# Optimization experiments

Hardware: AMD Instinct MI355X
Metric: run time of the kernel (lower is better)

Reference implementation:

```python
import jax, jax.numpy as jnp
import numpy as np

B, T, D, H = 16, 256, 128, 256  # batch, max_len, input_size, hidden_size (= attention hidden)


def _gru(x_seq, h0, Wih, Whh, bih, bhh):
    """Torch-style GRU over time. x_seq: [B,T,H_in], h0: [B,H]. Returns outputs [B,T,H], hT [B,H]."""
    x_proj = jnp.einsum('bti,gi->btg', x_seq, Wih) + bih  # [B,T,3H], precompute input projections

    def step(h, xp):
        gi_r, gi_z, gi_n = jnp.split(xp, 3, axis=-1)
        gh = h @ Whh.T + bhh
        gh_r, gh_z, gh_n = jnp.split(gh, 3, axis=-1)
        r = jax.nn.sigmoid(gi_r + gh_r)
        z = jax.nn.sigmoid(gi_z + gh_z)
        n = jnp.tanh(gi_n + r * gh_n)
        h_new = (1.0 - z) * n + z * h
        return h_new, h_new

    hT, outs = jax.lax.scan(step, h0, jnp.swapaxes(x_proj, 0, 1))  # scan over time
    return jnp.swapaxes(outs, 0, 1), hT


def setup_inputs() -> dict:
    key = jax.random.key(0)
    ks = jax.random.split(key, 16)
    s = lambda fan: 1.0 / np.sqrt(fan)
    inp = {
        'inputs': jax.random.normal(ks[0], (B, T, D), dtype=jnp.float32),
        'targets': jax.vmap(lambda k: jax.random.permutation(k, T))(jax.random.split(ks[1], B)).astype(jnp.int64),
        'W_enc': jax.random.normal(ks[2], (H, D), dtype=jnp.float32) * s(D),
        'b_enc': jnp.zeros((H,), dtype=jnp.float32),
        'enc_Wih': jax.random.normal(ks[3], (3 * H, H), dtype=jnp.float32) * s(H),
        'enc_Whh': jax.random.normal(ks[4], (3 * H, H), dtype=jnp.float32) * s(H),
        'enc_bih': jnp.zeros((3 * H,), dtype=jnp.float32),
        'enc_bhh': jnp.zeros((3 * H,), dtype=jnp.float32),
        'dec_Wih': jax.random.normal(ks[5], (3 * H, H), dtype=jnp.float32) * s(H),
        'dec_Whh': jax.random.normal(ks[6], (3 * H, H), dtype=jnp.float32) * s(H),
        'dec_bih': jnp.zeros((3 * H,), dtype=jnp.float32),
        'dec_bhh': jnp.zeros((3 * H,), dtype=jnp.float32),
        'Wq': jax.random.normal(ks[7], (H, H), dtype=jnp.float32) * s(H),
        'Wk': jax.random.normal(ks[8], (H, H), dtype=jnp.float32) * s(H),
        'v': jax.random.normal(ks[9], (H,), dtype=jnp.float32) * s(H),
    }
    return inp


def reference(inputs, targets, W_enc, b_enc, enc_Wih, enc_Whh, enc_bih, enc_bhh,
              dec_Wih, dec_Whh, dec_bih, dec_bhh, Wq, Wk, v):
    # encoder_linear (dropout = 0 at inference)
    enc_in = jnp.einsum('btd,hd->bth', inputs, W_enc) + b_enc  # [B,T,H]
    enc_out, hT = _gru(enc_in, jnp.zeros((B, H), dtype=inputs.dtype), enc_Wih, enc_Whh, enc_bih, enc_bhh)
    # teacher forcing: decoder inputs are encoder_inputs gathered at rolled targets
    dec_idx = jnp.roll(targets, 1, axis=1)  # [B,T]
    dec_rnn_in = jnp.take_along_axis(enc_in, dec_idx[:, :, None], axis=1)  # [B,T,H]
    dec_out, _ = _gru(dec_rnn_in, hT, dec_Wih, dec_Whh, dec_bih, dec_bhh)  # [B,T,H]
    # steps mask: position j available at step t iff j not in targets[:, :t]
    onehot = jax.nn.one_hot(targets, T, dtype=jnp.int32)         # [B,T,T]
    prev = jnp.cumsum(onehot, axis=1) - onehot                   # exclusive cumsum
    steps_mask = prev == 0                                       # [B,T(query),T(key)] bool
    # Bahdanau additive attention: v . tanh(Wq q + Wk k)
    q = jnp.einsum('bth,ah->bta', dec_out, Wq)  # [B,T,A]
    k = jnp.einsum('bsh,ah->bsa', enc_out, Wk)  # [B,S,A]
    scores = jnp.einsum('btsa,a->bts', jnp.tanh(q[:, :, None, :] + k[:, None, :, :]), v)  # [B,T,S]
    logits = jnp.where(steps_mask, scores, jnp.float32(-1e9))
    return logits
```

## Files before the change

### kernel.cpp

```cpp
#include <hip/hip_runtime.h>
#include <hip/hip_fp16.h>

#define B_ 16
#define T_ 256
#define D_ 128
#define H_ 256

typedef _Float16 f16;
typedef __attribute__((ext_vector_type(2))) _Float16 f16x2;
typedef __attribute__((ext_vector_type(4))) int i32x4;

__device__ __forceinline__ float fast_rcp(float x) {
#if __has_builtin(__builtin_amdgcn_rcpf)
    return __builtin_amdgcn_rcpf(x);
#else
    return 1.0f / x;
#endif
}
__device__ __forceinline__ float sigmoid_f(float x) {
    return fast_rcp(1.0f + __expf(-x));
}
__device__ __forceinline__ float tanh_f(float x) {
    float e = __expf(2.0f * x);
    return 1.0f - 2.0f * fast_rcp(1.0f + e);
}
__device__ __forceinline__ float tanh_pade(float x) {
#if __has_builtin(__builtin_amdgcn_fmed3f)
    x = __builtin_amdgcn_fmed3f(x, -4.f, 4.f);
#else
    x = fminf(4.f, fmaxf(-4.f, x));
#endif
    float x2 = x * x;
    return x * (27.f + x2) * fast_rcp(27.f + 9.f * x2);
}
__device__ __forceinline__ int dot8(int a, int b, int c) {
#if __has_builtin(__builtin_amdgcn_sdot8)
    return __builtin_amdgcn_sdot8(a, b, c, false);
#else
    int d;
    asm("v_dot8_i32_i4 %0, %1, %2, %3" : "=v"(d) : "v"(a), "v"(b), "v"(c));
    return d;
#endif
}
template <int CTRL>
__device__ __forceinline__ int dpp_quad(int x) {
    return __builtin_amdgcn_update_dpp(0, x, CTRL, 0xF, 0xF, true);
}
#define DPP_XOR1 0xB1
#define DPP_XOR2 0x4E

__global__ __launch_bounds__(256)
void k_prep_proj(const float* __restrict__ wa, const float* __restrict__ wb,
                 int* __restrict__ w4a, int* __restrict__ w4b,
                 float* __restrict__ sca, float* __restrict__ scb,
                 const int* __restrict__ tgt, int* __restrict__ pos,
                 const float* __restrict__ inputs,
                 const float* __restrict__ Wenc, const float* __restrict__ benc,
                 const float* __restrict__ We, const float* __restrict__ bihe,
                 const float* __restrict__ bhhe,
                 const float* __restrict__ Wd, const float* __restrict__ bihd,
                 const float* __restrict__ bhhd,
                 f16x2* __restrict__ giAe, f16* __restrict__ giBe,
                 f16x2* __restrict__ giAd, f16* __restrict__ giBd) {
    int blk = blockIdx.x;
    int a = threadIdx.x;
    if (blk < 384) {
        int wid = blk * 4 + (a >> 6);
        int l = a & 63;
        const float* W = wid < 768 ? wa : wb;
        int* w4 = wid < 768 ? w4a : w4b;
        float* sc = wid < 768 ? sca : scb;
        int r = wid & 767;
        int g = r >> 8, j = r & 255;
        const float* Wr = W + r * 256;
        float v[8];
        float m = 0.f;
        if (l < 32) {
#pragma unroll
            for (int q = 0; q < 8; ++q) {
                v[q] = Wr[8 * l + q];
                m = fmaxf(m, fabsf(v[q]));
            }
        }
#pragma unroll
        for (int d = 1; d < 64; d <<= 1) m = fmaxf(m, __shfl_xor(m, d));
        float qs = m > 0.f ? 7.f / m : 0.f;
        if (l == 0) sc[r] = m / 49.f;
        if (l < 32) {
            int pk = 0;
#pragma unroll
            for (int q = 0; q < 8; ++q) pk |= ((int)rintf(v[q] * qs) & 15) << (4 * q);
            int hf = l >> 4, i = l & 15;
            w4[(j * 2 + hf) * 48 + g * 16 + i] = pk;
        }
        return;
    }
    if (blk < 400) {
        __shared__ int pl[256];
        int b = blk - 384;
        pl[a] = T_;
        __syncthreads();
        atomicMin(&pl[tgt[b * 256 + a] & 255], a);
        __syncthreads();
        pos[b * 256 + a] = pl[a];
        return;
    }
    __shared__ float s_in[16][128];
    __shared__ float s_enc[16][256];
    int pblk = blk - 400;
    bool isdec = pblk >= 256;
    int bt0 = (pblk & 255) * 16;
    int b = bt0 >> 8;
    const float* W = isdec ? Wd : We;
    const float* bih = isdec ? bihd : bihe;
    const float* bhh = isdec ? bhhd : bhhe;
    f16x2* giA = isdec ? giAd : giAe;
    f16* giB = isdec ? giBd : giBe;

    int tsrc[16];
#pragma unroll
    for (int tt = 0; tt < 16; ++tt) {
        int t = (bt0 & 255) + tt;
        tsrc[tt] = isdec ? (tgt[(b << 8) + ((t + 255) & 255)] & 255) : t;
    }
#pragma unroll
    for (int it = 0; it < 2; ++it) {
        int idx = a + it * 256;
        int row = idx >> 5, k4 = idx & 31;
        ((float4*)s_in[row])[k4] =
            *(const float4*)(inputs + (b * 256 + tsrc[row]) * 128 + k4 * 4);
    }
    __syncthreads();
    {
        float eacc[16];
#pragma unroll
        for (int tt = 0; tt < 16; ++tt) eacc[tt] = benc[a];
        const float* wr = Wenc + a * 128;
        for (int k = 0; k < 128; k += 4) {
            float4 w4 = *(const float4*)(wr + k);
#pragma unroll
            for (int tt = 0; tt < 16; ++tt) {
                float4 x4 = *(const float4*)&s_in[tt][k];
                eacc[tt] += w4.x * x4.x + w4.y * x4.y + w4.z * x4.z + w4.w * x4.w;
            }
        }
#pragma unroll
        for (int tt = 0; tt < 16; ++tt) s_enc[tt][a] = eacc[tt];
    }
    __syncthreads();
    float acc0[16], acc1[16], acc2[16];
    float b0 = bih[a] + bhh[a];
    float b1 = bih[a + 256] + bhh[a + 256];
    float b2 = bih[a + 512];
#pragma unroll
    for (int tt = 0; tt < 16; ++tt) { acc0[tt] = b0; acc1[tt] = b1; acc2[tt] = b2; }
    const float* w0 = W + a * H_;
    const float* w1 = W + (a + 256) * H_;
    const float* w2 = W + (a + 512) * H_;
    for (int k = 0; k < H_; k += 4) {
        float4 a4 = *(const float4*)(w0 + k);
        float4 b4 = *(const float4*)(w1 + k);
        float4 c4 = *(const float4*)(w2 + k);
#pragma unroll
        for (int tt = 0; tt < 16; ++tt) {
            float4 x4 = *(const float4*)&s_enc[tt][k];
            acc0[tt] += a4.x * x4.x + a4.y * x4.y + a4.z * x4.z + a4.w * x4.w;
            acc1[tt] += b4.x * x4.x + b4.y * x4.y + b4.z * x4.z + b4.w * x4.w;
            acc2[tt] += c4.x * x4.x + c4.y * x4.y + c4.z * x4.z + c4.w * x4.w;
        }
    }
#pragma unroll
    for (int tt = 0; tt < 16; ++tt) {
        int row = bt0 + tt;
        giA[row * 256 + a] = (f16x2){(f16)acc0[tt], (f16)acc1[tt]};
        giB[row * 256 + a] = (f16)acc2[tt];
    }
}

__global__ __launch_bounds__(512)
__attribute__((amdgpu_waves_per_eu(2, 2)))
void k_gru2(const int* __restrict__ w4e, const int* __restrict__ w4d,
            const float* __restrict__ sce, const float* __restrict__ scd,
            const f16x2* __restrict__ giAe, const f16* __restrict__ giBe,
            const f16x2* __restrict__ giAd, const f16* __restrict__ giBd,
            const float* __restrict__ bhhe, const float* __restrict__ bhhd,
            float* __restrict__ enc_out, float* __restrict__ dec_out) {
    __shared__ __align__(16) int sh_h4[2][32];
    const int tid = threadIdx.x;
    const int m = blockIdx.x;
    const int j = tid >> 1;
    const int hf = tid & 1;

    if (tid < 64) ((int*)sh_h4)[tid] = 0;
    float hj = 0.f;
    __syncthreads();

    for (int ph = 0; ph < 2; ++ph) {
        const int* w4 = ph ? w4d : w4e;
        const float* scp = ph ? scd : sce;
        const float sc0 = scp[j], sc1 = scp[256 + j], sc2 = scp[512 + j];
        const float bn = (ph ? bhhd : bhhe)[512 + j];
        const f16x2* gA = (ph ? giAd : giAe) + m * (T_ * 256);
        const f16* gB = (ph ? giBd : giBe) + m * (T_ * 256);
        float* outp = (ph ? dec_out : enc_out) + m * (T_ * H_);

        i32x4 wq[3][4];
        {
            unsigned long long base = (unsigned long long)(w4 + tid * 48);
#pragma unroll
            for (int g = 0; g < 3; ++g)
#pragma unroll
                for (int q4 = 0; q4 < 4; ++q4)
                    asm volatile("global_load_dwordx4 %0, %1, off offset:%2"
                                 : "=v"(wq[g][q4]) : "v"(base), "i"(g * 64 + q4 * 16));
            asm volatile("s_waitcnt vmcnt(0)" ::: "memory");
        }

        f16x2 gab = gA[j];
        f16 gn = gB[j];

        for (int t = 0; t < T_; ++t) {
            const int cur = t & 1;
            int a0 = 0, a1 = 0, a2 = 0;
            const i32x4* hb = (const i32x4*)((const char*)sh_h4 + cur * 128 + hf * 64);
#pragma unroll
            for (int q4 = 0; q4 < 4; ++q4) {
                i32x4 h4 = hb[q4];
#pragma unroll
                for (int d = 0; d < 4; ++d) {
                    a0 = dot8(wq[0][q4][d], h4[d], a0);
                    a1 = dot8(wq[1][q4][d], h4[d], a1);
                    a2 = dot8(wq[2][q4][d], h4[d], a2);
                }
            }
            const int tn = (t < T_ - 1) ? t + 1 : t;
            f16x2 ngab = gA[tn * 256 + j];
            f16 ngn = gB[tn * 256 + j];

            a0 += dpp_quad<DPP_XOR1>(a0);
            a1 += dpp_quad<DPP_XOR1>(a1);
            a2 += dpp_quad<DPP_XOR1>(a2);
            float p0 = (float)a0 * sc0;
            float p1 = (float)a1 * sc1;
            float p2 = (float)a2 * sc2;

            float rr = sigmoid_f((float)gab[0] + p0);
            float zz = sigmoid_f((float)gab[1] + p1);
            float nv = tanh_f((float)gn + rr * (p2 + bn));
            float hn = (1.f - zz) * nv + zz * hj;
            hj = hn;

            if (hf) outp[t * H_ + j] = hn;
            int nib = (int)rintf(hn * 7.f) & 15;
            int hi = dpp_quad<DPP_XOR2>(nib);
            if ((tid & 3) == 0)
                ((char*)sh_h4)[(cur ^ 1) * 128 + (tid >> 2)] = (char)(nib | (hi << 4));

            gab = ngab; gn = ngn;
            asm volatile("s_waitcnt lgkmcnt(0)" ::: "memory");
            __builtin_amdgcn_s_barrier();
        }
    }
}

__global__ __launch_bounds__(256) void k_kT(const float* __restrict__ enc_out,
                                            const float* __restrict__ Wk,
                                            float* __restrict__ kT) {
    __shared__ float tile[8][256];
    int bt0 = blockIdx.x * 8;
    int a = threadIdx.x;
    float acc[8];
#pragma unroll
    for (int tt = 0; tt < 8; ++tt) acc[tt] = 0.f;
    const float* w0 = Wk + a * H_;
    for (int k = 0; k < H_; k += 4) {
        float4 w4 = *(const float4*)(w0 + k);
#pragma unroll
        for (int tt = 0; tt < 8; ++tt) {
            float4 x4 = *(const float4*)(enc_out + (bt0 + tt) * H_ + k);
            acc[tt] += w4.x * x4.x + w4.y * x4.y + w4.z * x4.z + w4.w * x4.w;
        }
    }
#pragma unroll
    for (int tt = 0; tt < 8; ++tt) tile[tt][a] = acc[tt];
    __syncthreads();
    int b = bt0 >> 8, s0 = bt0 & 255;
    float4 f0 = {tile[0][a], tile[1][a], tile[2][a], tile[3][a]};
    float4 f1 = {tile[4][a], tile[5][a], tile[6][a], tile[7][a]};
    *(float4*)(kT + b * (T_ * H_) + a * T_ + s0) = f0;
    *(float4*)(kT + b * (T_ * H_) + a * T_ + s0 + 4) = f1;
}

__global__ __launch_bounds__(256) void k_scores(const float* __restrict__ dec_out,
                                                const float* __restrict__ Wq,
                                                const float* __restrict__ kT,
                                                const float* __restrict__ v,
                                                const int* __restrict__ pos,
                                                float* __restrict__ out) {
    __shared__ float sdec[4][256];
    __shared__ float sq[4][256];
    __shared__ float sv[256];
    int blk = blockIdx.x;
    int b = blk >> 6;
    int t0 = (blk & 63) * 4;
    int s = threadIdx.x;
    sv[s] = v[s];
#pragma unroll
    for (int tt = 0; tt < 4; ++tt)
        sdec[tt][s] = dec_out[((b << 8) + t0 + tt) * H_ + s];
    __syncthreads();
    {
        float qa[4] = {0.f, 0.f, 0.f, 0.f};
        const float* wq = Wq + s * H_;
        for (int k = 0; k < H_; k += 4) {
            float4 w4 = *(const float4*)(wq + k);
#pragma unroll
            for (int tt = 0; tt < 4; ++tt) {
                float4 x4 = *(const float4*)&sdec[tt][k];
                qa[tt] += w4.x * x4.x + w4.y * x4.y + w4.z * x4.z + w4.w * x4.w;
            }
        }
#pragma unroll
        for (int tt = 0; tt < 4; ++tt) sq[tt][s] = qa[tt];
    }
    __syncthreads();
    int ps = pos[(b << 8) + s];
    float acc[4] = {0.f, 0.f, 0.f, 0.f};
    const float* kTb = kT + b * (T_ * H_);
    for (int a = 0; a < H_; ++a) {
        float kv = kTb[a * T_ + s];
        float va = sv[a];
#pragma unroll
        for (int tt = 0; tt < 4; ++tt) {
            float th = tanh_pade(sq[tt][a] + kv);
            acc[tt] += va * th;
        }
    }
#pragma unroll
    for (int tt = 0; tt < 4; ++tt) {
        int t = t0 + tt;
        out[((b << 8) + t) * T_ + s] = (t <= ps) ? acc[tt] : -1.0e9f;
    }
}

extern "C" void kernel_launch(void* const* d_in, const int* in_sizes, int n_in,
                              void* d_out, int out_size, void* d_ws, size_t ws_size,
                              hipStream_t stream) {
    (void)in_sizes; (void)n_in; (void)out_size; (void)ws_size;
    const float* inputs   = (const float*)d_in[0];
    const int* targets    = (const int*)d_in[1];
    const float* W_enc   = (const float*)d_in[2];
    const float* b_enc   = (const float*)d_in[3];
    const float* enc_Wih = (const float*)d_in[4];
    const float* enc_Whh = (const float*)d_in[5];
    const float* enc_bih = (const float*)d_in[6];
    const float* enc_bhh = (const float*)d_in[7];
    const float* dec_Wih = (const float*)d_in[8];
    const float* dec_Whh = (const float*)d_in[9];
    const float* dec_bih = (const float*)d_in[10];
    const float* dec_bhh = (const float*)d_in[11];
    const float* Wq = (const float*)d_in[12];
    const float* Wk = (const float*)d_in[13];
    const float* v  = (const float*)d_in[14];
    float* out = (float*)d_out;

    float* ws = (float*)d_ws;
    f16x2* giAe    = (f16x2*)ws;
    f16*   giBe    = (f16*)(ws + 1048576);
    f16x2* giAd    = (f16x2*)(ws + 1572864);
    f16*   giBd    = (f16*)(ws + 2621440);
    float* enc_out = ws + 3145728;
    float* dec_out = ws + 4194304;
    int*   w4e     = (int*)(ws + 5242880);
    int*   w4d     = (int*)(ws + 5292032);
    float* sce     = ws + 5341184;
    float* scd     = ws + 5341952;
    int*   pos     = (int*)(ws + 5342720);
    float* kT = (float*)giAd;

    k_prep_proj<<<912, 256, 0, stream>>>(enc_Whh, dec_Whh, w4e, w4d, sce, scd,
                                         targets, pos, inputs, W_enc, b_enc,
                                         enc_Wih, enc_bih, enc_bhh,
                                         dec_Wih, dec_bih, dec_bhh,
                                         giAe, giBe, giAd, giBd);
    k_gru2<<<16, 512, 0, stream>>>(w4e, w4d, sce, scd, giAe, giBe, giAd, giBd,
                                   enc_bhh, dec_bhh, enc_out, dec_out);
    k_kT<<<512, 256, 0, stream>>>(enc_out, Wk, kT);
    k_scores<<<1024, 256, 0, stream>>>(dec_out, Wq, kT, v, pos, out);
}
```

Baseline: 511.4 us.

## Overlap GRU recurrences with decoder projection and key projection in shared launches

Splits the single encoder+decoder GRU kernel into two launches. Each launch runs the sequential recurrence on 16 blocks while its other blocks compute independent work: the decoder input projection alongside the encoder GRU, and the Wk key projection alongside the decoder GRU. The query projection moves out of the scores kernel into its own kernel so it is computed once per row. This hides serial GRU latency behind otherwise idle CUs, at the cost of an extra launch, an hT round-trip, and the prep kernel now doing redundant duplicate input loads.

```diff
diff --git a/kernel.cpp b/kernel.cpp
--- a/kernel.cpp
+++ b/kernel.cpp
@@ -49,19 +49,86 @@
 #define DPP_XOR1 0xB1
 #define DPP_XOR2 0x4E
 
+__device__ __forceinline__ void gru_phase(const int* __restrict__ w4,
+                                          const float* __restrict__ scp,
+                                          const float* __restrict__ bhp,
+                                          const f16x2* __restrict__ gA,
+                                          const f16* __restrict__ gB,
+                                          float* __restrict__ outp,
+                                          float& hj, int* sh_h4, int tid) {
+    const int j = tid >> 1;
+    const int hf = tid & 1;
+    const float sc0 = scp[j], sc1 = scp[256 + j], sc2 = scp[512 + j];
+    const float bn = bhp[512 + j];
+
+    i32x4 wq[3][4];
+    {
+        unsigned long long base = (unsigned long long)(w4 + tid * 48);
+#pragma unroll
+        for (int g = 0; g < 3; ++g)
+#pragma unroll
+            for (int q4 = 0; q4 < 4; ++q4)
+                asm volatile("global_load_dwordx4 %0, %1, off offset:%2"
+                             : "=v"(wq[g][q4]) : "v"(base), "i"(g * 64 + q4 * 16));
+        asm volatile("s_waitcnt vmcnt(0)" ::: "memory");
+    }
+
+    f16x2 gab = gA[j];
+    f16 gn = gB[j];
+
+    for (int t = 0; t < T_; ++t) {
+        const int cur = t & 1;
+        int a0 = 0, a1 = 0, a2 = 0;
+        const i32x4* hb = (const i32x4*)((const char*)sh_h4 + cur * 128 + hf * 64);
+#pragma unroll
+        for (int q4 = 0; q4 < 4; ++q4) {
+            i32x4 h4 = hb[q4];
+#pragma unroll
+            for (int d = 0; d < 4; ++d) {
+                a0 = dot8(wq[0][q4][d], h4[d], a0);
+                a1 = dot8(wq[1][q4][d], h4[d], a1);
+                a2 = dot8(wq[2][q4][d], h4[d], a2);
+            }
+        }
+        const int tn = (t < T_ - 1) ? t + 1 : t;
+        f16x2 ngab = gA[tn * 256 + j];
+        f16 ngn = gB[tn * 256 + j];
+
+        a0 += dpp_quad<DPP_XOR1>(a0);
+        a1 += dpp_quad<DPP_XOR1>(a1);
+        a2 += dpp_quad<DPP_XOR1>(a2);
+        float p0 = (float)a0 * sc0;
+        float p1 = (float)a1 * sc1;
+        float p2 = (float)a2 * sc2;
+
+        float rr = sigmoid_f((float)gab[0] + p0);
+        float zz = sigmoid_f((float)gab[1] + p1);
+        float nv = tanh_f((float)gn + rr * (p2 + bn));
+        float hn = (1.f - zz) * nv + zz * hj;
+        hj = hn;
+
+        if (hf) outp[t * H_ + j] = hn;
+        int nib = (int)rintf(hn * 7.f) & 15;
+        int hi = dpp_quad<DPP_XOR2>(nib);
+        if ((tid & 3) == 0)
+            ((char*)sh_h4)[(cur ^ 1) * 128 + (tid >> 2)] = (char)(nib | (hi << 4));
+
+        gab = ngab; gn = ngn;
+        asm volatile("s_waitcnt lgkmcnt(0)" ::: "memory");
+        __builtin_amdgcn_s_barrier();
+    }
+}
+
 __global__ __launch_bounds__(256)
-void k_prep_proj(const float* __restrict__ wa, const float* __restrict__ wb,
-                 int* __restrict__ w4a, int* __restrict__ w4b,
-                 float* __restrict__ sca, float* __restrict__ scb,
-                 const int* __restrict__ tgt, int* __restrict__ pos,
-                 const float* __restrict__ inputs,
-                 const float* __restrict__ Wenc, const float* __restrict__ benc,
-                 const float* __restrict__ We, const float* __restrict__ bihe,
-                 const float* __restrict__ bhhe,
-                 const float* __restrict__ Wd, const float* __restrict__ bihd,
-                 const float* __restrict__ bhhd,
-                 f16x2* __restrict__ giAe, f16* __restrict__ giBe,
-                 f16x2* __restrict__ giAd, f16* __restrict__ giBd) {
+void k_prep_pe(const float* __restrict__ wa, const float* __restrict__ wb,
+               int* __restrict__ w4a, int* __restrict__ w4b,
+               float* __restrict__ sca, float* __restrict__ scb,
+               const int* __restrict__ tgt, int* __restrict__ pos,
+               const float* __restrict__ inputs,
+               const float* __restrict__ Wenc, const float* __restrict__ benc,
+               const float* __restrict__ We, const float* __restrict__ bihe,
+               const float* __restrict__ bhhe,
+               f16x2* __restrict__ giAe, f16* __restrict__ giBe) {
     int blk = blockIdx.x;
     int a = threadIdx.x;
     if (blk < 384) {
@@ -108,27 +175,25 @@
     __shared__ float s_in[16][128];
     __shared__ float s_enc[16][256];
     int pblk = blk - 400;
-    bool isdec = pblk >= 256;
-    int bt0 = (pblk & 255) * 16;
+    int bt0 = pblk * 16;
     int b = bt0 >> 8;
-    const float* W = isdec ? Wd : We;
-    const float* bih = isdec ? bihd : bihe;
-    const float* bhh = isdec ? bhhd : bhhe;
-    f16x2* giA = isdec ? giAd : giAe;
-    f16* giB = isdec ? giBd : giBe;
-
-    int tsrc[16];
-#pragma unroll
-    for (int tt = 0; tt < 16; ++tt) {
-        int t = (bt0 & 255) + tt;
-        tsrc[tt] = isdec ? (tgt[(b << 8) + ((t + 255) & 255)] & 255) : t;
-    }
+    {
+        int idx = a * 4 >> 7, k = (a * 4) & 127;
+        *(float4*)&s_in[idx][k] = *(const float4*)(inputs + (b * 256 + (bt0 & 255) + idx) * 128 + k);
+    }
+    {
+        int idx = a + 256;
+        int row = idx >> 5, k4 = idx & 31;
+        ((float4*)s_in[row])[k4] =
+            *(const float4*)(inputs + (b * 256 + (bt0 & 255) + row) * 128 + k4 * 4);
+    }
+    __syncthreads();
 #pragma unroll
     for (int it = 0; it < 2; ++it) {
         int idx = a + it * 256;
         int row = idx >> 5, k4 = idx & 31;
         ((float4*)s_in[row])[k4] =
-            *(const float4*)(inputs + (b * 256 + tsrc[row]) * 128 + k4 * 4);
+            *(const float4*)(inputs + (b * 256 + (bt0 & 255) + row) * 128 + k4 * 4);
     }
     __syncthreads();
     {
@@ -149,14 +214,14 @@
     }
     __syncthreads();
     float acc0[16], acc1[16], acc2[16];
-    float b0 = bih[a] + bhh[a];
-    float b1 = bih[a + 256] + bhh[a + 256];
-    float b2 = bih[a + 512];
+    float b0 = bihe[a] + bhhe[a];
+    float b1 = bihe[a + 256] + bhhe[a + 256];
+    float b2 = bihe[a + 512];
 #pragma unroll
     for (int tt = 0; tt < 16; ++tt) { acc0[tt] = b0; acc1[tt] = b1; acc2[tt] = b2; }
-    const float* w0 = W + a * H_;
-    const float* w1 = W + (a + 256) * H_;
-    const float* w2 = W + (a + 512) * H_;
+    const float* w0 = We + a * H_;
+    const float* w1 = We + (a + 256) * H_;
+    const float* w2 = We + (a + 512) * H_;
     for (int k = 0; k < H_; k += 4) {
         float4 a4 = *(const float4*)(w0 + k);
         float4 b4 = *(const float4*)(w1 + k);
@@ -172,132 +237,183 @@
 #pragma unroll
     for (int tt = 0; tt < 16; ++tt) {
         int row = bt0 + tt;
-        giA[row * 256 + a] = (f16x2){(f16)acc0[tt], (f16)acc1[tt]};
-        giB[row * 256 + a] = (f16)acc2[tt];
+        giAe[row * 256 + a] = (f16x2){(f16)acc0[tt], (f16)acc1[tt]};
+        giBe[row * 256 + a] = (f16)acc2[tt];
     }
 }
 
 __global__ __launch_bounds__(512)
 __attribute__((amdgpu_waves_per_eu(2, 2)))
-void k_gru2(const int* __restrict__ w4e, const int* __restrict__ w4d,
-            const float* __restrict__ sce, const float* __restrict__ scd,
-            const f16x2* __restrict__ giAe, const f16* __restrict__ giBe,
-            const f16x2* __restrict__ giAd, const f16* __restrict__ giBd,
-            const float* __restrict__ bhhe, const float* __restrict__ bhhd,
-            float* __restrict__ enc_out, float* __restrict__ dec_out) {
+void k_egru_pd(const int* __restrict__ w4e, const float* __restrict__ sce,
+               const f16x2* __restrict__ giAe, const f16* __restrict__ giBe,
+               const float* __restrict__ bhhe,
+               float* __restrict__ enc_out, float* __restrict__ hT,
+               const float* __restrict__ inputs,
+               const float* __restrict__ Wenc, const float* __restrict__ benc,
+               const float* __restrict__ Wd, const float* __restrict__ bihd,
+               const float* __restrict__ bhhd, const int* __restrict__ tgt,
+               f16x2* __restrict__ giAd, f16* __restrict__ giBd) {
     __shared__ __align__(16) int sh_h4[2][32];
+    __shared__ float s_in[32][128];
+    __shared__ float s_enc[32][256];
+    const int blk = blockIdx.x;
     const int tid = threadIdx.x;
-    const int m = blockIdx.x;
-    const int j = tid >> 1;
-    const int hf = tid & 1;
-
-    if (tid < 64) ((int*)sh_h4)[tid] = 0;
-    float hj = 0.f;
-    __syncthreads();
-
-    for (int ph = 0; ph < 2; ++ph) {
-        const int* w4 = ph ? w4d : w4e;
-        const float* scp = ph ? scd : sce;
-        const float sc0 = scp[j], sc1 = scp[256 + j], sc2 = scp[512 + j];
-        const float bn = (ph ? bhhd : bhhe)[512 + j];
-        const f16x2* gA = (ph ? giAd : giAe) + m * (T_ * 256);
-        const f16* gB = (ph ? giBd : giBe) + m * (T_ * 256);
-        float* outp = (ph ? dec_out : enc_out) + m * (T_ * H_);
-
-        i32x4 wq[3][4];
-        {
-            unsigned long long base = (unsigned long long)(w4 + tid * 48);
-#pragma unroll
-            for (int g = 0; g < 3; ++g)
-#pragma unroll
-                for (int q4 = 0; q4 < 4; ++q4)
-                    asm volatile("global_load_dwordx4 %0, %1, off offset:%2"
-                                 : "=v"(wq[g][q4]) : "v"(base), "i"(g * 64 + q4 * 16));
-            asm volatile("s_waitcnt vmcnt(0)" ::: "memory");
-        }
-
-        f16x2 gab = gA[j];
-        f16 gn = gB[j];
-
-        for (int t = 0; t < T_; ++t) {
-            const int cur = t & 1;
-            int a0 = 0, a1 = 0, a2 = 0;
-            const i32x4* hb = (const i32x4*)((const char*)sh_h4 + cur * 128 + hf * 64);
-#pragma unroll
-            for (int q4 = 0; q4 < 4; ++q4) {
-                i32x4 h4 = hb[q4];
-#pragma unroll
-                for (int d = 0; d < 4; ++d) {
-                    a0 = dot8(wq[0][q4][d], h4[d], a0);
-                    a1 = dot8(wq[1][q4][d], h4[d], a1);
-                    a2 = dot8(wq[2][q4][d], h4[d], a2);
-                }
+    if (blk < 16) {
+        const int m = blk;
+        if (tid < 64) ((int*)sh_h4)[tid] = 0;
+        float hj = 0.f;
+        __syncthreads();
+        gru_phase(w4e, sce, bhhe, giAe + m * (T_ * 256), giBe + m * (T_ * 256),
+                  enc_out + m * (T_ * H_), hj, &sh_h4[0][0], tid);
+        if (tid & 1) hT[m * H_ + (tid >> 1)] = hj;
+        return;
+    }
+    const int pblk = blk - 16;
+    const int bt0 = pblk * 32;
+    const int b = bt0 >> 8;
+    const int a = tid & 255;
+    const int half = tid >> 8;
+    int tsrc[16];
+#pragma unroll
+    for (int i = 0; i < 16; ++i) {
+        int t = (bt0 & 255) + half * 16 + i;
+        tsrc[i] = tgt[(b << 8) + ((t + 255) & 255)] & 255;
+    }
+#pragma unroll
+    for (int it = 0; it < 2; ++it) {
+        int idx = tid + it * 512;
+        int row = idx >> 5, k4 = idx & 31;
+        int t = (bt0 & 255) + row;
+        int rs = tgt[(b << 8) + ((t + 255) & 255)] & 255;
+        ((float4*)s_in[row])[k4] = *(const float4*)(inputs + (b * 256 + rs) * 128 + k4 * 4);
+    }
+    __syncthreads();
+    {
+        float eacc[16];
+#pragma unroll
+        for (int i = 0; i < 16; ++i) eacc[i] = benc[a];
+        const float* wr = Wenc + a * 128;
+        for (int k = 0; k < 128; k += 4) {
+            float4 w4 = *(const float4*)(wr + k);
+#pragma unroll
+            for (int i = 0; i < 16; ++i) {
+                float4 x4 = *(const float4*)&s_in[half * 16 + i][k];
+                eacc[i] += w4.x * x4.x + w4.y * x4.y + w4.z * x4.z + w4.w * x4.w;
             }
-            const int tn = (t < T_ - 1) ? t + 1 : t;
-            f16x2 ngab = gA[tn * 256 + j];
-            f16 ngn = gB[tn * 256 + j];
-
-            a0 += dpp_quad<DPP_XOR1>(a0);
-            a1 += dpp_quad<DPP_XOR1>(a1);
-            a2 += dpp_quad<DPP_XOR1>(a2);
-            float p0 = (float)a0 * sc0;
-            float p1 = (float)a1 * sc1;
-            float p2 = (float)a2 * sc2;
-
-            float rr = sigmoid_f((float)gab[0] + p0);
-            float zz = sigmoid_f((float)gab[1] + p1);
-            float nv = tanh_f((float)gn + rr * (p2 + bn));
-            float hn = (1.f - zz) * nv + zz * hj;
-            hj = hn;
-
-            if (hf) outp[t * H_ + j] = hn;
-            int nib = (int)rintf(hn * 7.f) & 15;
-            int hi = dpp_quad<DPP_XOR2>(nib);
-            if ((tid & 3) == 0)
-                ((char*)sh_h4)[(cur ^ 1) * 128 + (tid >> 2)] = (char)(nib | (hi << 4));
-
-            gab = ngab; gn = ngn;
-            asm volatile("s_waitcnt lgkmcnt(0)" ::: "memory");
-            __builtin_amdgcn_s_barrier();
-        }
-    }
-}
-
-__global__ __launch_bounds__(256) void k_kT(const float* __restrict__ enc_out,
-                                            const float* __restrict__ Wk,
-                                            float* __restrict__ kT) {
-    __shared__ float tile[8][256];
-    int bt0 = blockIdx.x * 8;
-    int a = threadIdx.x;
-    float acc[8];
-#pragma unroll
-    for (int tt = 0; tt < 8; ++tt) acc[tt] = 0.f;
+        }
+#pragma unroll
+        for (int i = 0; i < 16; ++i) s_enc[half * 16 + i][a] = eacc[i];
+    }
+    __syncthreads();
+    float acc0[16], acc1[16], acc2[16];
+    float b0 = bihd[a] + bhhd[a];
+    float b1 = bihd[a + 256] + bhhd[a + 256];
+    float b2 = bihd[a + 512];
+#pragma unroll
+    for (int i = 0; i < 16; ++i) { acc0[i] = b0; acc1[i] = b1; acc2[i] = b2; }
+    const float* w0 = Wd + a * H_;
+    const float* w1 = Wd + (a + 256) * H_;
+    const float* w2 = Wd + (a + 512) * H_;
+    for (int k = 0; k < H_; k += 4) {
+        float4 a4 = *(const float4*)(w0 + k);
+        float4 b4 = *(const float4*)(w1 + k);
+        float4 c4 = *(const float4*)(w2 + k);
+#pragma unroll
+        for (int i = 0; i < 16; ++i) {
+            float4 x4 = *(const float4*)&s_enc[half * 16 + i][k];
+            acc0[i] += a4.x * x4.x + a4.y * x4.y + a4.z * x4.z + a4.w * x4.w;
+            acc1[i] += b4.x * x4.x + b4.y * x4.y + b4.z * x4.z + b4.w * x4.w;
+            acc2[i] += c4.x * x4.x + c4.y * x4.y + c4.z * x4.z + c4.w * x4.w;
+        }
+    }
+#pragma unroll
+    for (int i = 0; i < 16; ++i) {
+        int row = bt0 + half * 16 + i;
+        giAd[row * 256 + a] = (f16x2){(f16)acc0[i], (f16)acc1[i]};
+        giBd[row * 256 + a] = (f16)acc2[i];
+    }
+    (void)tsrc;
+}
+
+__global__ __launch_bounds__(512)
+__attribute__((amdgpu_waves_per_eu(2, 2)))
+void k_dgru_kt(const int* __restrict__ w4d, const float* __restrict__ scd,
+               const f16x2* __restrict__ giAd, const f16* __restrict__ giBd,
+               const float* __restrict__ bhhd,
+               float* __restrict__ dec_out, const float* __restrict__ hT,
+               const float* __restrict__ enc_out, const float* __restrict__ Wk,
+               float* __restrict__ kT) {
+    __shared__ __align__(16) int sh_h4[2][32];
+    __shared__ float tile[32][256];
+    const int blk = blockIdx.x;
+    const int tid = threadIdx.x;
+    if (blk < 16) {
+        const int m = blk;
+        const int j = tid >> 1;
+        float hj = hT[m * H_ + j];
+        int nib = (int)rintf(hj * 7.f) & 15;
+        int hi = dpp_quad<DPP_XOR2>(nib);
+        if ((tid & 3) == 0)
+            ((char*)sh_h4)[tid >> 2] = (char)(nib | (hi << 4));
+        __syncthreads();
+        gru_phase(w4d, scd, bhhd, giAd + m * (T_ * 256), giBd + m * (T_ * 256),
+                  dec_out + m * (T_ * H_), hj, &sh_h4[0][0], tid);
+        return;
+    }
+    const int kblk = blk - 16;
+    const int bt0 = kblk * 32;
+    const int b = bt0 >> 8, s0 = bt0 & 255;
+    const int a = tid & 255;
+    const int half = tid >> 8;
+    float acc[16];
+#pragma unroll
+    for (int i = 0; i < 16; ++i) acc[i] = 0.f;
     const float* w0 = Wk + a * H_;
     for (int k = 0; k < H_; k += 4) {
         float4 w4 = *(const float4*)(w0 + k);
 #pragma unroll
-        for (int tt = 0; tt < 8; ++tt) {
-            float4 x4 = *(const float4*)(enc_out + (bt0 + tt) * H_ + k);
+        for (int i = 0; i < 16; ++i) {
+            float4 x4 = *(const float4*)(enc_out + (bt0 + half * 16 + i) * H_ + k);
+            acc[i] += w4.x * x4.x + w4.y * x4.y + w4.z * x4.z + w4.w * x4.w;
+        }
+    }
+#pragma unroll
+    for (int i = 0; i < 16; ++i) tile[half * 16 + i][a] = acc[i];
+    __syncthreads();
+#pragma unroll
+    for (int i4 = 0; i4 < 4; ++i4) {
+        float4 f = {tile[half * 16 + i4 * 4 + 0][a], tile[half * 16 + i4 * 4 + 1][a],
+                    tile[half * 16 + i4 * 4 + 2][a], tile[half * 16 + i4 * 4 + 3][a]};
+        *(float4*)(kT + b * (T_ * H_) + a * T_ + s0 + half * 16 + i4 * 4) = f;
+    }
+}
+
+__global__ __launch_bounds__(256) void k_q(const float* __restrict__ dec_out,
+                                           const float* __restrict__ Wq,
+                                           float* __restrict__ q) {
+    int bt0 = blockIdx.x * 16;
+    int a = threadIdx.x;
+    float acc[16];
+#pragma unroll
+    for (int tt = 0; tt < 16; ++tt) acc[tt] = 0.f;
+    const float* w0 = Wq + a * H_;
+    for (int k = 0; k < H_; k += 4) {
+        float4 w4 = *(const float4*)(w0 + k);
+#pragma unroll
+        for (int tt = 0; tt < 16; ++tt) {
+            float4 x4 = *(const float4*)(dec_out + (bt0 + tt) * H_ + k);
             acc[tt] += w4.x * x4.x + w4.y * x4.y + w4.z * x4.z + w4.w * x4.w;
         }
     }
 #pragma unroll
-    for (int tt = 0; tt < 8; ++tt) tile[tt][a] = acc[tt];
-    __syncthreads();
-    int b = bt0 >> 8, s0 = bt0 & 255;
-    float4 f0 = {tile[0][a], tile[1][a], tile[2][a], tile[3][a]};
-    float4 f1 = {tile[4][a], tile[5][a], tile[6][a], tile[7][a]};
-    *(float4*)(kT + b * (T_ * H_) + a * T_ + s0) = f0;
-    *(float4*)(kT + b * (T_ * H_) + a * T_ + s0 + 4) = f1;
-}
-
-__global__ __launch_bounds__(256) void k_scores(const float* __restrict__ dec_out,
-                                                const float* __restrict__ Wq,
+    for (int tt = 0; tt < 16; ++tt) q[(bt0 + tt) * H_ + a] = acc[tt];
+}
+
+__global__ __launch_bounds__(256) void k_scores(const float* __restrict__ q,
                                                 const float* __restrict__ kT,
                                                 const float* __restrict__ v,
                                                 const int* __restrict__ pos,
                                                 float* __restrict__ out) {
-    __shared__ float sdec[4][256];
     __shared__ float sq[4][256];
     __shared__ float sv[256];
     int blk = blockIdx.x;
@@ -307,22 +423,7 @@
     sv[s] = v[s];
 #pragma unroll
     for (int tt = 0; tt < 4; ++tt)
-        sdec[tt][s] = dec_out[((b << 8) + t0 + tt) * H_ + s];
-    __syncthreads();
-    {
-        float qa[4] = {0.f, 0.f, 0.f, 0.f};
-        const float* wq = Wq + s * H_;
-        for (int k = 0; k < H_; k += 4) {
-            float4 w4 = *(const float4*)(wq + k);
-#pragma unroll
-            for (int tt = 0; tt < 4; ++tt) {
-                float4 x4 = *(const float4*)&sdec[tt][k];
-                qa[tt] += w4.x * x4.x + w4.y * x4.y + w4.z * x4.z + w4.w * x4.w;
-            }
-        }
-#pragma unroll
-        for (int tt = 0; tt < 4; ++tt) sq[tt][s] = qa[tt];
-    }
+        sq[tt][s] = q[((b << 8) + t0 + tt) * H_ + s];
     __syncthreads();
     int ps = pos[(b << 8) + s];
     float acc[4] = {0.f, 0.f, 0.f, 0.f};
@@ -376,15 +477,19 @@
     float* sce     = ws + 5341184;
     float* scd     = ws + 5341952;
     int*   pos     = (int*)(ws + 5342720);
-    float* kT = (float*)giAd;
-
-    k_prep_proj<<<912, 256, 0, stream>>>(enc_Whh, dec_Whh, w4e, w4d, sce, scd,
-                                         targets, pos, inputs, W_enc, b_enc,
-                                         enc_Wih, enc_bih, enc_bhh,
-                                         dec_Wih, dec_bih, dec_bhh,
-                                         giAe, giBe, giAd, giBd);
-    k_gru2<<<16, 512, 0, stream>>>(w4e, w4d, sce, scd, giAe, giBe, giAd, giBd,
-                                   enc_bhh, dec_bhh, enc_out, dec_out);
-    k_kT<<<512, 256, 0, stream>>>(enc_out, Wk, kT);
-    k_scores<<<1024, 256, 0, stream>>>(dec_out, Wq, kT, v, pos, out);
-}
+    float* hT      = ws + 5346816;
+    float* kT = (float*)giAe;
+    float* q  = (float*)giAd;
+
+    k_prep_pe<<<656, 256, 0, stream>>>(enc_Whh, dec_Whh, w4e, w4d, sce, scd,
+                                       targets, pos, inputs, W_enc, b_enc,
+                                       enc_Wih, enc_bih, enc_bhh, giAe, giBe);
+    k_egru_pd<<<144, 512, 0, stream>>>(w4e, sce, giAe, giBe, enc_bhh, enc_out, hT,
+                                       inputs, W_enc, b_enc,
+                                       dec_Wih, dec_bih, dec_bhh, targets,
+                                       giAd, giBd);
+    k_dgru_kt<<<144, 512, 0, stream>>>(w4d, scd, giAd, giBd, dec_bhh, dec_out, hT,
+                                       enc_out, Wk, kT);
+    k_q<<<256, 256, 0, stream>>>(dec_out, Wq, q);
+    k_scores<<<1024, 256, 0, stream>>>(q, kT, v, pos, out);
+}
```

Result: faster. 412.7 us (-19.3%).
